# Performance work log

Hardware: AMD Instinct MI355X
Metric: run time of the kernel (lower is better)

## Reference

```python
import jax, jax.numpy as jnp
import numpy as np

EMBED_DIM = 512
NUM_HEADS = 8
DEPTH = EMBED_DIM // NUM_HEADS
B, S = 2, 4096


def setup_inputs() -> dict:
    key = jax.random.key(0)
    ks = jax.random.split(key, 11)
    s = 1.0 / np.sqrt(EMBED_DIM)
    return {
        "q": jax.random.normal(ks[0], (B, S, EMBED_DIM), jnp.float32),
        "k": jax.random.normal(ks[1], (B, S, EMBED_DIM), jnp.float32),
        "v": jax.random.normal(ks[2], (B, S, EMBED_DIM), jnp.float32),
        "mask": jnp.zeros((B, 1, 1, S), jnp.float32),  # additive mask: 1=masked, 0=keep
        "Wq": jax.random.normal(ks[3], (EMBED_DIM, EMBED_DIM), jnp.float32) * s,
        "bq": jnp.zeros((EMBED_DIM,), jnp.float32),
        "Wk": jax.random.normal(ks[4], (EMBED_DIM, EMBED_DIM), jnp.float32) * s,
        "bk": jnp.zeros((EMBED_DIM,), jnp.float32),
        "Wv": jax.random.normal(ks[5], (EMBED_DIM, EMBED_DIM), jnp.float32) * s,
        "bv": jnp.zeros((EMBED_DIM,), jnp.float32),
        "Wo": jax.random.normal(ks[6], (EMBED_DIM, EMBED_DIM), jnp.float32) * s,
        "bo": jnp.zeros((EMBED_DIM,), jnp.float32),
    }


def _split_heads(x):
    b, s, _ = x.shape
    return x.reshape(b, s, NUM_HEADS, DEPTH).transpose(0, 2, 1, 3)  # [B,H,S,D]


def reference(q, k, v, mask, Wq, bq, Wk, bk, Wv, bv, Wo, bo):
    qh = _split_heads(q @ Wq + bq)
    kh = _split_heads(k @ Wk + bk)
    vh = _split_heads(v @ Wv + bv)
    logits = jnp.einsum("bhqd,bhkd->bhqk", qh, kh) / jnp.sqrt(jnp.float32(DEPTH))
    logits = logits + mask * -1e9
    attn = jax.nn.softmax(logits, axis=-1)
    out = jnp.einsum("bhqk,bhkd->bhqd", attn, vh)
    out = out.transpose(0, 2, 1, 3).reshape(q.shape[0], -1, EMBED_DIM)
    return out @ Wo + bo
```

## Files before the change

### kernel.cpp

```cpp
#include <hip/hip_runtime.h>
#include <stdint.h>

typedef __bf16 bf16;
typedef bf16 bf16x8 __attribute__((ext_vector_type(8)));
typedef float f32x4 __attribute__((ext_vector_type(4)));
typedef float f32x16 __attribute__((ext_vector_type(16)));

#define EMBED 512
#define NHEAD 8
#define DEPTH 64
#define BATCH 2
#define SEQ 4096
#define M_TOTAL (BATCH * SEQ)
#define KVH 2048
#define NT (KVH / 64)

#define LOG2E 1.44269504f
#define QSCALE (0.125f * LOG2E)
#define MASKC (-1.0e9f * LOG2E)
#define DEFER_THR 10.0f

__device__ __forceinline__ void gload16(const void* g, void* l) {
  __builtin_amdgcn_global_load_lds((const __attribute__((address_space(1))) unsigned*)g,
                                   (__attribute__((address_space(3))) unsigned*)l, 16, 0, 0);
}
__device__ __forceinline__ uint32_t cvtpk(float a, float b) {
  uint32_t r;
  asm volatile("v_cvt_pk_bf16_f32 %0, %1, %2" : "=v"(r) : "v"(a), "v"(b));
  return r;
}
__device__ __forceinline__ void plswap(uint32_t& a, uint32_t& b) {
  asm volatile("v_permlane32_swap_b32 %0, %1" : "+v"(a), "+v"(b));
}
__device__ __forceinline__ float vdup(float x) {
  float r;
  asm volatile("v_mov_b32 %0, %1" : "=v"(r) : "v"(x));
  return r;
}
__device__ __forceinline__ float cross_max(float x) {
  float a = x, b = vdup(x);
  asm volatile("v_permlane32_swap_b32 %0, %1" : "+v"(a), "+v"(b));
  return fmaxf(a, b);
}
__device__ __forceinline__ float cross_sum(float x) {
  float a = x, b = vdup(x);
  asm volatile("v_permlane32_swap_b32 %0, %1" : "+v"(a), "+v"(b));
  return a + b;
}
union U4 { uint32_t u[4]; bf16x8 v; };

__global__ __launch_bounds__(256) void cvt3(const float* __restrict__ q, const float* __restrict__ k,
                                            const float* __restrict__ v, bf16* __restrict__ oq,
                                            bf16* __restrict__ ok, bf16* __restrict__ ov) {
  int z = blockIdx.y;
  const float* in = z == 0 ? q : (z == 1 ? k : v);
  bf16* out = z == 0 ? oq : (z == 1 ? ok : ov);
  size_t i = ((size_t)blockIdx.x * 256 + threadIdx.x) * 8;
  float4 f0 = *(const float4*)(in + i);
  float4 f1 = *(const float4*)(in + i + 4);
  bf16x8 o;
  o[0] = (bf16)f0.x; o[1] = (bf16)f0.y; o[2] = (bf16)f0.z; o[3] = (bf16)f0.w;
  o[4] = (bf16)f1.x; o[5] = (bf16)f1.y; o[6] = (bf16)f1.z; o[7] = (bf16)f1.w;
  *(bf16x8*)(out + i) = o;
}

__global__ __launch_bounds__(256) void transpose4(const float* __restrict__ W0, const float* __restrict__ W1,
                                                  const float* __restrict__ W2, const float* __restrict__ W3,
                                                  bf16* __restrict__ T0, bf16* __restrict__ T1,
                                                  bf16* __restrict__ T2, bf16* __restrict__ T3) {
  int z = blockIdx.z;
  const float* W = z == 0 ? W0 : (z == 1 ? W1 : (z == 2 ? W2 : W3));
  bf16* WT = z == 0 ? T0 : (z == 1 ? T1 : (z == 2 ? T2 : T3));
  __shared__ float t[32][33];
  int k0 = blockIdx.x * 32, n0 = blockIdx.y * 32;
  int x = threadIdx.x & 31, y = threadIdx.x >> 5;
#pragma unroll
  for (int yy = y; yy < 32; yy += 8)
    t[yy][x] = W[(size_t)(k0 + yy) * EMBED + n0 + x];
  __syncthreads();
#pragma unroll
  for (int yy = y; yy < 32; yy += 8)
    WT[(size_t)(n0 + yy) * EMBED + k0 + x] = (bf16)t[x][yy];
}

__device__ __forceinline__ void gemm128_body(const bf16* __restrict__ A, const bf16* __restrict__ Bt,
                                             const float* __restrict__ bias, void* __restrict__ out,
                                             float scale, int mode) {
  __shared__ __align__(16) bf16 As[128 * 64];
  __shared__ __align__(16) bf16 Bs[128 * 64];
  int tid = threadIdx.x, lane = tid & 63, w = tid >> 6;
  int g = lane >> 4, r = lane & 15;
  int n0 = blockIdx.x * 128, m0 = blockIdx.y * 128;
  int wr = (w >> 1) * 64, wc = (w & 1) * 64;

  f32x4 acc[4][4];
#pragma unroll
  for (int m = 0; m < 4; m++)
#pragma unroll
    for (int n = 0; n < 4; n++)
#pragma unroll
      for (int i = 0; i < 4; i++) acc[m][n][i] = 0.f;

  size_t aoff[4], boff[4];
#pragma unroll
  for (int i = 0; i < 4; i++) {
    int u = w * 64 + lane + i * 256;
    int row = u >> 3, scs = (u & 7) ^ (row & 7);
    aoff[i] = (size_t)(m0 + row) * EMBED + scs * 8;
    boff[i] = (size_t)(n0 + row) * EMBED + scs * 8;
  }

  for (int k0 = 0; k0 < EMBED; k0 += 64) {
#pragma unroll
    for (int i = 0; i < 4; i++) {
      gload16(A + aoff[i] + k0, &As[(w + i * 4) * 512]);
      gload16(Bt + boff[i] + k0, &Bs[(w + i * 4) * 512]);
    }
    __syncthreads();
#pragma unroll
    for (int kk = 0; kk < 64; kk += 32) {
      bf16x8 af[4], bf_[4];
#pragma unroll
      for (int m = 0; m < 4; m++) {
        int row = wr + m * 16 + r;
        af[m] = *(const bf16x8*)&As[row * 64 + (((kk >> 3) + g) ^ (r & 7)) * 8];
      }
#pragma unroll
      for (int n = 0; n < 4; n++) {
        int col = wc + n * 16 + r;
        bf_[n] = *(const bf16x8*)&Bs[col * 64 + (((kk >> 3) + g) ^ (r & 7)) * 8];
      }
      __builtin_amdgcn_s_setprio(1);
#pragma unroll
      for (int m = 0; m < 4; m++)
#pragma unroll
        for (int n = 0; n < 4; n++)
          acc[m][n] = __builtin_amdgcn_mfma_f32_16x16x32_bf16(af[m], bf_[n], acc[m][n], 0, 0, 0);
      __builtin_amdgcn_s_setprio(0);
    }
    __syncthreads();
  }

#pragma unroll
  for (int n = 0; n < 4; n++) {
    int ncol = n0 + wc + n * 16 + r;
    float bv = bias[ncol];
#pragma unroll
    for (int m = 0; m < 4; m++)
#pragma unroll
      for (int v_ = 0; v_ < 4; v_++) {
        int mrow = m0 + wr + m * 16 + g * 4 + v_;
        float val = (acc[m][n][v_] + bv) * scale;
        if (mode == 2) {
          ((float*)out)[(size_t)mrow * EMBED + ncol] = val;
        } else {
          int b = mrow >> 12, s = mrow & (SEQ - 1);
          int h = ncol >> 6, d = ncol & 63;
          size_t idx = (mode == 0) ? ((((size_t)(b * NHEAD + h)) * SEQ + s) * DEPTH + d)
                                   : ((((size_t)(b * NHEAD + h)) * DEPTH + d) * SEQ + s);
          ((bf16*)out)[idx] = (bf16)val;
        }
      }
  }
}

__global__ __launch_bounds__(256, 2) void gemm_qkv(const bf16* __restrict__ Xq, const bf16* __restrict__ Xk,
                                                   const bf16* __restrict__ Xv, const bf16* __restrict__ Tq,
                                                   const bf16* __restrict__ Tk, const bf16* __restrict__ Tv,
                                                   const float* __restrict__ bq, const float* __restrict__ bk,
                                                   const float* __restrict__ bv, bf16* __restrict__ qh,
                                                   bf16* __restrict__ kh, bf16* __restrict__ vT) {
  int z = blockIdx.z;
  const bf16* A = z == 0 ? Xq : (z == 1 ? Xk : Xv);
  const bf16* Bt = z == 0 ? Tq : (z == 1 ? Tk : Tv);
  const float* bias = z == 0 ? bq : (z == 1 ? bk : bv);
  void* out = z == 0 ? (void*)qh : (z == 1 ? (void*)kh : (void*)vT);
  float scale = z == 0 ? QSCALE : 1.0f;
  int mode = z == 2 ? 1 : 0;
  gemm128_body(A, Bt, bias, out, scale, mode);
}

__global__ __launch_bounds__(256, 2) void gemm_o(const bf16* __restrict__ A, const bf16* __restrict__ Bt,
                                                 const float* __restrict__ bias, float* __restrict__ out) {
  gemm128_body(A, Bt, bias, out, 1.0f, 2);
}

__global__ __launch_bounds__(512, 2) void flash_attn(const bf16* __restrict__ qh,
                                                     const bf16* __restrict__ kh,
                                                     const bf16* __restrict__ vT,
                                                     const float* __restrict__ mask,
                                                     bf16* __restrict__ O) {
  __shared__ __align__(16) unsigned char smem[65536];
  __shared__ float Sm[4][64];
  __shared__ float Sl[4][64];
  bf16* KV = (bf16*)smem;

  int tid = threadIdx.x;
  int lane = tid & 63, w = tid >> 6;
  int l31 = lane & 31, hi = lane >> 5, l7 = lane & 7;
  int qs = w & 3, half = w >> 2;
  int bh = blockIdx.y, b = bh >> 3, h = bh & 7;
  int q0 = blockIdx.x * 256;
  const bf16* Qb = qh + (size_t)bh * SEQ * DEPTH;
  const bf16* Kb = kh + (size_t)bh * SEQ * DEPTH;
  const bf16* Vb = vT + (size_t)bh * DEPTH * SEQ;
  const float* maskb = mask + (size_t)b * SEQ + half * KVH;

  int srow = tid >> 3;
  int scs = (tid & 7) ^ (srow & 7);
  const bf16* kg0 = Kb + (size_t)srow * DEPTH + scs * 8;
  const bf16* vg0 = Vb + (size_t)srow * SEQ + scs * 8;
  int wofs = w * 512;

#define STAGE(buf, kv)                                                              \
  do {                                                                              \
    gload16(kg0 + (size_t)(kv)*DEPTH, KV + (buf)*16384 + wofs);                     \
    gload16(kg0 + (size_t)((kv) + KVH) * DEPTH, KV + (buf)*16384 + 4096 + wofs);    \
    gload16(vg0 + (kv), KV + (buf)*16384 + 8192 + wofs);                            \
    gload16(vg0 + ((kv) + KVH), KV + (buf)*16384 + 12288 + wofs);                   \
  } while (0)

  STAGE(0, 0);

  bf16x8 qf[2][4];
#pragma unroll
  for (int q2 = 0; q2 < 2; q2++) {
    const bf16* qp = Qb + (size_t)(q0 + qs * 64 + q2 * 32 + l31) * DEPTH + hi * 8;
#pragma unroll
    for (int s = 0; s < 4; s++) qf[q2][s] = *(const bf16x8*)(qp + s * 16);
  }

  f32x16 oacc[2][2];
#pragma unroll
  for (int q2 = 0; q2 < 2; q2++)
#pragma unroll
    for (int nb = 0; nb < 2; nb++)
#pragma unroll
      for (int i = 0; i < 16; i++) oacc[q2][nb][i] = 0.f;
  float mrun[2] = {-__builtin_inff(), -__builtin_inff()};
  float lrun[2] = {0.f, 0.f};

  __syncthreads();

  int cur = 0;
  for (int t = 0; t < NT; ++t) {
    int kv = t * 64;
    if (t + 1 < NT) STAGE(cur ^ 1, kv + 64);

    const bf16* Kcur = KV + cur * 16384 + half * 4096;
    const bf16* Vcur = KV + cur * 16384 + 8192 + half * 4096;

    f32x4 mf[2][4];
#pragma unroll
    for (int m2 = 0; m2 < 2; m2++)
#pragma unroll
      for (int g = 0; g < 4; g++)
        mf[m2][g] = *(const f32x4*)(maskb + kv + m2 * 32 + g * 8 + 4 * hi);

    bf16x8 kf[2][4];
#pragma unroll
    for (int m2 = 0; m2 < 2; m2++)
#pragma unroll
      for (int s = 0; s < 4; s++)
        kf[m2][s] = *(const bf16x8*)(Kcur + (m2 * 32 + l31) * 64 + (((s * 2 + hi) ^ l7) * 8));

    bf16x8 pa[2][4];
#pragma unroll
    for (int q2 = 0; q2 < 2; q2++) {
      f32x16 sacc[2];
#pragma unroll
      for (int m2 = 0; m2 < 2; m2++)
#pragma unroll
        for (int i = 0; i < 16; i++) sacc[m2][i] = 0.f;
      __builtin_amdgcn_s_setprio(1);
#pragma unroll
      for (int m2 = 0; m2 < 2; m2++)
#pragma unroll
        for (int s = 0; s < 4; s++)
          sacc[m2] = __builtin_amdgcn_mfma_f32_32x32x16_bf16(kf[m2][s], qf[q2][s], sacc[m2], 0, 0, 0);
      __builtin_amdgcn_s_setprio(0);

#pragma unroll
      for (int m2 = 0; m2 < 2; m2++)
#pragma unroll
        for (int g = 0; g < 4; g++)
#pragma unroll
          for (int i = 0; i < 4; i++)
            sacc[m2][4 * g + i] = fmaf(mf[m2][g][i], MASKC, sacc[m2][4 * g + i]);

      float tmx[16];
#pragma unroll
      for (int i = 0; i < 16; i++) tmx[i] = fmaxf(sacc[0][i], sacc[1][i]);
#pragma unroll
      for (int i = 0; i < 8; i++) tmx[i] = fmaxf(tmx[i], tmx[i + 8]);
#pragma unroll
      for (int i = 0; i < 4; i++) tmx[i] = fmaxf(tmx[i], tmx[i + 4]);
      float pmax = fmaxf(fmaxf(tmx[0], tmx[1]), fmaxf(tmx[2], tmx[3]));
      pmax = cross_max(pmax);

      if (__any(pmax > mrun[q2] + DEFER_THR)) {
        float mnew = fmaxf(mrun[q2], pmax);
        float alpha = exp2f(mrun[q2] - mnew);
        lrun[q2] *= alpha;
        mrun[q2] = mnew;
#pragma unroll
        for (int r = 0; r < 16; r++) {
          float af = __shfl(alpha, (r & 3) + 8 * (r >> 2) + 4 * hi);
          oacc[q2][0][r] *= af;
          oacc[q2][1][r] *= af;
        }
      }

      float p[32];
      float rsv[4] = {0.f, 0.f, 0.f, 0.f};
#pragma unroll
      for (int m2 = 0; m2 < 2; m2++)
#pragma unroll
        for (int i = 0; i < 16; i++) {
          float pv = __builtin_amdgcn_exp2f(sacc[m2][i] - mrun[q2]);
          p[m2 * 16 + i] = pv;
          rsv[i & 3] += pv;
        }
      float rsum = (rsv[0] + rsv[1]) + (rsv[2] + rsv[3]);
      lrun[q2] += cross_sum(rsum);

#pragma unroll
      for (int m2 = 0; m2 < 2; m2++) {
        uint32_t c0 = cvtpk(p[m2 * 16 + 0], p[m2 * 16 + 1]);
        uint32_t c1 = cvtpk(p[m2 * 16 + 2], p[m2 * 16 + 3]);
        uint32_t d0 = cvtpk(p[m2 * 16 + 4], p[m2 * 16 + 5]);
        uint32_t d1 = cvtpk(p[m2 * 16 + 6], p[m2 * 16 + 7]);
        plswap(c0, d0);
        plswap(c1, d1);
        U4 e; e.u[0] = c0; e.u[1] = c1; e.u[2] = d0; e.u[3] = d1;
        pa[q2][m2 * 2 + 0] = e.v;
        uint32_t c2 = cvtpk(p[m2 * 16 + 8], p[m2 * 16 + 9]);
        uint32_t c3 = cvtpk(p[m2 * 16 + 10], p[m2 * 16 + 11]);
        uint32_t d2 = cvtpk(p[m2 * 16 + 12], p[m2 * 16 + 13]);
        uint32_t d3 = cvtpk(p[m2 * 16 + 14], p[m2 * 16 + 15]);
        plswap(c2, d2);
        plswap(c3, d3);
        U4 o; o.u[0] = c2; o.u[1] = c3; o.u[2] = d2; o.u[3] = d3;
        pa[q2][m2 * 2 + 1] = o.v;
      }
    }

    __builtin_amdgcn_s_setprio(1);
#pragma unroll
    for (int nb = 0; nb < 2; nb++)
#pragma unroll
      for (int ks = 0; ks < 4; ks++) {
        bf16x8 vf = *(const bf16x8*)(Vcur + (nb * 32 + l31) * 64 + (((ks * 2 + hi) ^ l7) * 8));
        oacc[0][nb] = __builtin_amdgcn_mfma_f32_32x32x16_bf16(pa[0][ks], vf, oacc[0][nb], 0, 0, 0);
        oacc[1][nb] = __builtin_amdgcn_mfma_f32_32x32x16_bf16(pa[1][ks], vf, oacc[1][nb], 0, 0, 0);
      }
    __builtin_amdgcn_s_setprio(0);

    __syncthreads();
    cur ^= 1;
  }

  float* Oex = (float*)smem;
  if (half == 1) {
    if (hi == 0) {
#pragma unroll
      for (int q2 = 0; q2 < 2; q2++) {
        Sm[qs][q2 * 32 + l31] = mrun[q2];
        Sl[qs][q2 * 32 + l31] = lrun[q2];
      }
    }
    float* Op = Oex + qs * 4096;
#pragma unroll
    for (int q2 = 0; q2 < 2; q2++)
#pragma unroll
      for (int nb = 0; nb < 2; nb++)
#pragma unroll
        for (int r = 0; r < 16; r++) {
          int cr = (r & 3) + 8 * (r >> 2) + 4 * hi;
          Op[(q2 * 32 + cr) * 64 + nb * 32 + l31] = oacc[q2][nb][r];
        }
  }
  __syncthreads();
  if (half == 0) {
    float s0[2], s1[2];
#pragma unroll
    for (int q2 = 0; q2 < 2; q2++) {
      float m1 = Sm[qs][q2 * 32 + l31];
      float l1 = Sl[qs][q2 * 32 + l31];
      float mm = fmaxf(mrun[q2], m1);
      float e0 = exp2f(mrun[q2] - mm);
      float e1 = exp2f(m1 - mm);
      float inv = 1.0f / (lrun[q2] * e0 + l1 * e1);
      s0[q2] = e0 * inv;
      s1[q2] = e1 * inv;
    }
    float* Op = Oex + qs * 4096;
    bf16* Ob = O + ((size_t)(b * SEQ + q0 + qs * 64)) * EMBED + h * DEPTH + l31;
#pragma unroll
    for (int q2 = 0; q2 < 2; q2++)
#pragma unroll
      for (int nb = 0; nb < 2; nb++)
#pragma unroll
        for (int r = 0; r < 16; r++) {
          int cr = (r & 3) + 8 * (r >> 2) + 4 * hi;
          float a0 = __shfl(s0[q2], cr);
          float a1 = __shfl(s1[q2], cr);
          float o1 = Op[(q2 * 32 + cr) * 64 + nb * 32 + l31];
          Ob[(size_t)(q2 * 32 + cr) * EMBED + nb * 32] = (bf16)(oacc[q2][nb][r] * a0 + o1 * a1);
        }
  }
#undef STAGE
}

extern "C" void kernel_launch(void* const* d_in, const int* in_sizes, int n_in,
                              void* d_out, int out_size, void* d_ws, size_t ws_size,
                              hipStream_t stream) {
  (void)in_sizes; (void)n_in; (void)out_size; (void)ws_size;
  const float* q = (const float*)d_in[0];
  const float* k = (const float*)d_in[1];
  const float* v = (const float*)d_in[2];
  const float* mask = (const float*)d_in[3];
  const float* Wq = (const float*)d_in[4];
  const float* bq = (const float*)d_in[5];
  const float* Wk = (const float*)d_in[6];
  const float* bk = (const float*)d_in[7];
  const float* Wv = (const float*)d_in[8];
  const float* bv = (const float*)d_in[9];
  const float* Wo = (const float*)d_in[10];
  const float* bo = (const float*)d_in[11];

  const size_t NX = (size_t)M_TOTAL * EMBED;
  const size_t NW = (size_t)EMBED * EMBED;
  bf16* Xq = (bf16*)d_ws;
  bf16* Xk = Xq + NX;
  bf16* Xv = Xk + NX;
  bf16* WTq = Xv + NX;
  bf16* WTk = WTq + NW;
  bf16* WTv = WTk + NW;
  bf16* WTo = WTv + NW;
  bf16* qh = WTo + NW;
  bf16* kh = qh + NX;
  bf16* vT = kh + NX;
  bf16* Ow = vT + NX;

  cvt3<<<dim3(NX / 2048, 3), 256, 0, stream>>>(q, k, v, Xq, Xk, Xv);
  transpose4<<<dim3(16, 16, 4), 256, 0, stream>>>(Wq, Wk, Wv, Wo, WTq, WTk, WTv, WTo);

  gemm_qkv<<<dim3(EMBED / 128, M_TOTAL / 128, 3), 256, 0, stream>>>(
      Xq, Xk, Xv, WTq, WTk, WTv, bq, bk, bv, qh, kh, vT);

  flash_attn<<<dim3(SEQ / 256, BATCH * NHEAD), 512, 0, stream>>>(qh, kh, vT, mask, Ow);

  gemm_o<<<dim3(EMBED / 128, M_TOTAL / 128), 256, 0, stream>>>(Ow, WTo, bo, (float*)d_out);
}
```

Before: 251.9 us.

## Restructure flash attention to single KV pass per block, fuse prep kernels, remap blocks

Flash attention drops the split-KV design (two halves of 4 waves each merged via shared memory). Each block now has 4 waves walking the full sequence, with a 32KB double buffer unrolled into a templated tile step, mask folded into the MFMA accumulator init, and a simple final normalisation. Launch bounds move to 256 threads with 4 blocks per CU. The input cast and weight transpose kernels are fused into one launch, and GEMM and attention block indices are swizzled so neighbouring blocks spread across XCDs. The trade-off is twice as many KV iterations per wave against removing the cross-half merge, gaining occupancy and saving one launch.

```diff
diff --git a/kernel.cpp b/kernel.cpp
--- a/kernel.cpp
+++ b/kernel.cpp
@@ -12,8 +12,6 @@
 #define BATCH 2
 #define SEQ 4096
 #define M_TOTAL (BATCH * SEQ)
-#define KVH 2048
-#define NT (KVH / 64)
 
 #define LOG2E 1.44269504f
 #define QSCALE (0.125f * LOG2E)
@@ -47,40 +45,46 @@
   asm volatile("v_permlane32_swap_b32 %0, %1" : "+v"(a), "+v"(b));
   return a + b;
 }
+__device__ __forceinline__ float max3f(float a, float b, float c) {
+  return fmaxf(fmaxf(a, b), c);
+}
 union U4 { uint32_t u[4]; bf16x8 v; };
 
-__global__ __launch_bounds__(256) void cvt3(const float* __restrict__ q, const float* __restrict__ k,
+__global__ __launch_bounds__(256) void prep(const float* __restrict__ q, const float* __restrict__ k,
                                             const float* __restrict__ v, bf16* __restrict__ oq,
-                                            bf16* __restrict__ ok, bf16* __restrict__ ov) {
+                                            bf16* __restrict__ ok, bf16* __restrict__ ov,
+                                            const float* __restrict__ W0, const float* __restrict__ W1,
+                                            const float* __restrict__ W2, const float* __restrict__ W3,
+                                            bf16* __restrict__ T0, bf16* __restrict__ T1,
+                                            bf16* __restrict__ T2, bf16* __restrict__ T3) {
+  __shared__ float t[32][33];
   int z = blockIdx.y;
-  const float* in = z == 0 ? q : (z == 1 ? k : v);
-  bf16* out = z == 0 ? oq : (z == 1 ? ok : ov);
-  size_t i = ((size_t)blockIdx.x * 256 + threadIdx.x) * 8;
-  float4 f0 = *(const float4*)(in + i);
-  float4 f1 = *(const float4*)(in + i + 4);
-  bf16x8 o;
-  o[0] = (bf16)f0.x; o[1] = (bf16)f0.y; o[2] = (bf16)f0.z; o[3] = (bf16)f0.w;
-  o[4] = (bf16)f1.x; o[5] = (bf16)f1.y; o[6] = (bf16)f1.z; o[7] = (bf16)f1.w;
-  *(bf16x8*)(out + i) = o;
-}
-
-__global__ __launch_bounds__(256) void transpose4(const float* __restrict__ W0, const float* __restrict__ W1,
-                                                  const float* __restrict__ W2, const float* __restrict__ W3,
-                                                  bf16* __restrict__ T0, bf16* __restrict__ T1,
-                                                  bf16* __restrict__ T2, bf16* __restrict__ T3) {
-  int z = blockIdx.z;
-  const float* W = z == 0 ? W0 : (z == 1 ? W1 : (z == 2 ? W2 : W3));
-  bf16* WT = z == 0 ? T0 : (z == 1 ? T1 : (z == 2 ? T2 : T3));
-  __shared__ float t[32][33];
-  int k0 = blockIdx.x * 32, n0 = blockIdx.y * 32;
-  int x = threadIdx.x & 31, y = threadIdx.x >> 5;
-#pragma unroll
-  for (int yy = y; yy < 32; yy += 8)
-    t[yy][x] = W[(size_t)(k0 + yy) * EMBED + n0 + x];
-  __syncthreads();
-#pragma unroll
-  for (int yy = y; yy < 32; yy += 8)
-    WT[(size_t)(n0 + yy) * EMBED + k0 + x] = (bf16)t[x][yy];
+  if (z < 3) {
+    const float* in = z == 0 ? q : (z == 1 ? k : v);
+    bf16* out = z == 0 ? oq : (z == 1 ? ok : ov);
+    size_t i = ((size_t)blockIdx.x * 256 + threadIdx.x) * 8;
+    float4 f0 = *(const float4*)(in + i);
+    float4 f1 = *(const float4*)(in + i + 4);
+    bf16x8 o;
+    o[0] = (bf16)f0.x; o[1] = (bf16)f0.y; o[2] = (bf16)f0.z; o[3] = (bf16)f0.w;
+    o[4] = (bf16)f1.x; o[5] = (bf16)f1.y; o[6] = (bf16)f1.z; o[7] = (bf16)f1.w;
+    *(bf16x8*)(out + i) = o;
+  } else {
+    int bx = blockIdx.x;
+    if (bx >= 1024) return;
+    int wsel = bx >> 8, rem = bx & 255;
+    const float* W = wsel == 0 ? W0 : (wsel == 1 ? W1 : (wsel == 2 ? W2 : W3));
+    bf16* WT = wsel == 0 ? T0 : (wsel == 1 ? T1 : (wsel == 2 ? T2 : T3));
+    int k0 = (rem >> 4) * 32, n0 = (rem & 15) * 32;
+    int x = threadIdx.x & 31, y = threadIdx.x >> 5;
+#pragma unroll
+    for (int yy = y; yy < 32; yy += 8)
+      t[yy][x] = W[(size_t)(k0 + yy) * EMBED + n0 + x];
+    __syncthreads();
+#pragma unroll
+    for (int yy = y; yy < 32; yy += 8)
+      WT[(size_t)(n0 + yy) * EMBED + k0 + x] = (bf16)t[x][yy];
+  }
 }
 
 __device__ __forceinline__ void gemm128_body(const bf16* __restrict__ A, const bf16* __restrict__ Bt,
@@ -90,7 +94,9 @@
   __shared__ __align__(16) bf16 Bs[128 * 64];
   int tid = threadIdx.x, lane = tid & 63, w = tid >> 6;
   int g = lane >> 4, r = lane & 15;
-  int n0 = blockIdx.x * 128, m0 = blockIdx.y * 128;
+  int orig = blockIdx.y * gridDim.x + blockIdx.x;
+  int wid = (orig & 7) * 32 + (orig >> 3);
+  int n0 = (wid & 3) * 128, m0 = (wid >> 2) * 128;
   int wr = (w >> 1) * 64, wc = (w & 1) * 64;
 
   f32x4 acc[4][4];
@@ -185,47 +191,157 @@
   gemm128_body(A, Bt, bias, out, 1.0f, 2);
 }
 
-__global__ __launch_bounds__(512, 2) void flash_attn(const bf16* __restrict__ qh,
+template <int BUF>
+__device__ __forceinline__ void tile_step(const char* rb, const int (&va)[4],
+                                          const bf16* kg0, const bf16* vg0, char* kvb,
+                                          const float* maskb, int kv, bool stage_next,
+                                          const bf16x8 (&qf)[2][4], f32x16 (&oacc)[2][2],
+                                          float (&mrun)[2], float (&lrun)[2], int hi) {
+  if (stage_next) {
+    int nkv = kv + 64;
+    gload16(kg0 + (size_t)nkv * DEPTH, kvb + (BUF ^ 1) * 8192);
+    gload16(kg0 + (size_t)(nkv + 32) * DEPTH, kvb + (BUF ^ 1) * 8192 + 4096);
+    gload16(vg0 + nkv, kvb + 16384 + (BUF ^ 1) * 8192);
+    gload16(vg0 + 32 * SEQ + nkv, kvb + 16384 + (BUF ^ 1) * 8192 + 4096);
+  }
+  f32x16 minit[2];
+#pragma unroll
+  for (int m2 = 0; m2 < 2; m2++)
+#pragma unroll
+    for (int g = 0; g < 4; g++) {
+      f32x4 f = *(const f32x4*)(maskb + kv + m2 * 32 + g * 8 + 4 * hi);
+#pragma unroll
+      for (int i = 0; i < 4; i++) minit[m2][4 * g + i] = f[i] * MASKC;
+    }
+  bf16x8 kf[2][4];
+#pragma unroll
+  for (int m2 = 0; m2 < 2; m2++)
+#pragma unroll
+    for (int s = 0; s < 4; s++)
+      kf[m2][s] = *(const bf16x8*)(rb + va[s] + BUF * 8192 + m2 * 4096);
+
+  bf16x8 pa[2][4];
+#pragma unroll
+  for (int q2 = 0; q2 < 2; q2++) {
+    f32x16 s0 = minit[0], s1 = minit[1];
+    __builtin_amdgcn_s_setprio(1);
+#pragma unroll
+    for (int s = 0; s < 4; s++) {
+      s0 = __builtin_amdgcn_mfma_f32_32x32x16_bf16(kf[0][s], qf[q2][s], s0, 0, 0, 0);
+      s1 = __builtin_amdgcn_mfma_f32_32x32x16_bf16(kf[1][s], qf[q2][s], s1, 0, 0, 0);
+    }
+    __builtin_amdgcn_s_setprio(0);
+
+    float mx[16];
+#pragma unroll
+    for (int i = 0; i < 16; i++) mx[i] = fmaxf(s0[i], s1[i]);
+    float u0 = max3f(mx[0], mx[1], mx[2]);
+    float u1 = max3f(mx[3], mx[4], mx[5]);
+    float u2 = max3f(mx[6], mx[7], mx[8]);
+    float u3 = max3f(mx[9], mx[10], mx[11]);
+    float u4 = max3f(mx[12], mx[13], mx[14]);
+    float pmax = fmaxf(max3f(u0, u1, u2), max3f(u3, u4, mx[15]));
+    pmax = cross_max(pmax);
+
+    if (__any(pmax > mrun[q2] + DEFER_THR)) {
+      float mnew = fmaxf(mrun[q2], pmax);
+      float alpha = exp2f(mrun[q2] - mnew);
+      lrun[q2] *= alpha;
+      mrun[q2] = mnew;
+#pragma unroll
+      for (int r = 0; r < 16; r++) {
+        float af = __shfl(alpha, (r & 3) + 8 * (r >> 2) + 4 * hi);
+        oacc[q2][0][r] *= af;
+        oacc[q2][1][r] *= af;
+      }
+    }
+
+    float p[32];
+    float rsv[4] = {0.f, 0.f, 0.f, 0.f};
+#pragma unroll
+    for (int i = 0; i < 16; i++) {
+      p[i] = __builtin_amdgcn_exp2f(s0[i] - mrun[q2]);
+      rsv[i & 3] += p[i];
+    }
+#pragma unroll
+    for (int i = 0; i < 16; i++) {
+      p[16 + i] = __builtin_amdgcn_exp2f(s1[i] - mrun[q2]);
+      rsv[i & 3] += p[16 + i];
+    }
+    lrun[q2] += cross_sum((rsv[0] + rsv[1]) + (rsv[2] + rsv[3]));
+
+#pragma unroll
+    for (int m2 = 0; m2 < 2; m2++) {
+      uint32_t c0 = cvtpk(p[m2 * 16 + 0], p[m2 * 16 + 1]);
+      uint32_t c1 = cvtpk(p[m2 * 16 + 2], p[m2 * 16 + 3]);
+      uint32_t d0 = cvtpk(p[m2 * 16 + 4], p[m2 * 16 + 5]);
+      uint32_t d1 = cvtpk(p[m2 * 16 + 6], p[m2 * 16 + 7]);
+      plswap(c0, d0);
+      plswap(c1, d1);
+      U4 e; e.u[0] = c0; e.u[1] = c1; e.u[2] = d0; e.u[3] = d1;
+      pa[q2][m2 * 2 + 0] = e.v;
+      uint32_t c2 = cvtpk(p[m2 * 16 + 8], p[m2 * 16 + 9]);
+      uint32_t c3 = cvtpk(p[m2 * 16 + 10], p[m2 * 16 + 11]);
+      uint32_t d2 = cvtpk(p[m2 * 16 + 12], p[m2 * 16 + 13]);
+      uint32_t d3 = cvtpk(p[m2 * 16 + 14], p[m2 * 16 + 15]);
+      plswap(c2, d2);
+      plswap(c3, d3);
+      U4 o; o.u[0] = c2; o.u[1] = c3; o.u[2] = d2; o.u[3] = d3;
+      pa[q2][m2 * 2 + 1] = o.v;
+    }
+  }
+
+  __builtin_amdgcn_s_setprio(1);
+#pragma unroll
+  for (int nb = 0; nb < 2; nb++)
+#pragma unroll
+    for (int ks = 0; ks < 4; ks++) {
+      bf16x8 vf = *(const bf16x8*)(rb + va[ks] + 16384 + BUF * 8192 + nb * 4096);
+      oacc[0][nb] = __builtin_amdgcn_mfma_f32_32x32x16_bf16(pa[0][ks], vf, oacc[0][nb], 0, 0, 0);
+      oacc[1][nb] = __builtin_amdgcn_mfma_f32_32x32x16_bf16(pa[1][ks], vf, oacc[1][nb], 0, 0, 0);
+    }
+  __builtin_amdgcn_s_setprio(0);
+  __syncthreads();
+}
+
+__global__ __launch_bounds__(256, 4) void flash_attn(const bf16* __restrict__ qh,
                                                      const bf16* __restrict__ kh,
                                                      const bf16* __restrict__ vT,
                                                      const float* __restrict__ mask,
                                                      bf16* __restrict__ O) {
-  __shared__ __align__(16) unsigned char smem[65536];
-  __shared__ float Sm[4][64];
-  __shared__ float Sl[4][64];
-  bf16* KV = (bf16*)smem;
-
-  int tid = threadIdx.x;
-  int lane = tid & 63, w = tid >> 6;
+  __shared__ __align__(16) unsigned char smem[32768];
+  int tid = threadIdx.x, lane = tid & 63, w = tid >> 6;
   int l31 = lane & 31, hi = lane >> 5, l7 = lane & 7;
-  int qs = w & 3, half = w >> 2;
-  int bh = blockIdx.y, b = bh >> 3, h = bh & 7;
-  int q0 = blockIdx.x * 256;
+  int orig = blockIdx.y * 16 + blockIdx.x;
+  int wid = (orig & 7) * 32 + (orig >> 3);
+  int qblk = wid & 15, bh = wid >> 4;
+  int b = bh >> 3, h = bh & 7;
+  int q0 = qblk * 256;
   const bf16* Qb = qh + (size_t)bh * SEQ * DEPTH;
   const bf16* Kb = kh + (size_t)bh * SEQ * DEPTH;
   const bf16* Vb = vT + (size_t)bh * DEPTH * SEQ;
-  const float* maskb = mask + (size_t)b * SEQ + half * KVH;
+  const float* maskb = mask + (size_t)b * SEQ;
 
   int srow = tid >> 3;
   int scs = (tid & 7) ^ (srow & 7);
   const bf16* kg0 = Kb + (size_t)srow * DEPTH + scs * 8;
   const bf16* vg0 = Vb + (size_t)srow * SEQ + scs * 8;
-  int wofs = w * 512;
-
-#define STAGE(buf, kv)                                                              \
-  do {                                                                              \
-    gload16(kg0 + (size_t)(kv)*DEPTH, KV + (buf)*16384 + wofs);                     \
-    gload16(kg0 + (size_t)((kv) + KVH) * DEPTH, KV + (buf)*16384 + 4096 + wofs);    \
-    gload16(vg0 + (kv), KV + (buf)*16384 + 8192 + wofs);                            \
-    gload16(vg0 + ((kv) + KVH), KV + (buf)*16384 + 12288 + wofs);                   \
-  } while (0)
-
-  STAGE(0, 0);
+  char* kvb = (char*)smem + w * 1024;
+  const char* rb = (const char*)smem;
+
+  int va[4];
+#pragma unroll
+  for (int s = 0; s < 4; s++) va[s] = l31 * 128 + (((s * 2 + hi) ^ l7) * 16);
+
+  gload16(kg0, kvb);
+  gload16(kg0 + (size_t)32 * DEPTH, kvb + 4096);
+  gload16(vg0, kvb + 16384);
+  gload16(vg0 + 32 * SEQ, kvb + 16384 + 4096);
 
   bf16x8 qf[2][4];
 #pragma unroll
   for (int q2 = 0; q2 < 2; q2++) {
-    const bf16* qp = Qb + (size_t)(q0 + qs * 64 + q2 * 32 + l31) * DEPTH + hi * 8;
+    const bf16* qp = Qb + (size_t)(q0 + w * 64 + q2 * 32 + l31) * DEPTH + hi * 8;
 #pragma unroll
     for (int s = 0; s < 4; s++) qf[q2][s] = *(const bf16x8*)(qp + s * 16);
   }
@@ -242,174 +358,24 @@
 
   __syncthreads();
 
-  int cur = 0;
-  for (int t = 0; t < NT; ++t) {
-    int kv = t * 64;
-    if (t + 1 < NT) STAGE(cur ^ 1, kv + 64);
-
-    const bf16* Kcur = KV + cur * 16384 + half * 4096;
-    const bf16* Vcur = KV + cur * 16384 + 8192 + half * 4096;
-
-    f32x4 mf[2][4];
-#pragma unroll
-    for (int m2 = 0; m2 < 2; m2++)
-#pragma unroll
-      for (int g = 0; g < 4; g++)
-        mf[m2][g] = *(const f32x4*)(maskb + kv + m2 * 32 + g * 8 + 4 * hi);
-
-    bf16x8 kf[2][4];
-#pragma unroll
-    for (int m2 = 0; m2 < 2; m2++)
-#pragma unroll
-      for (int s = 0; s < 4; s++)
-        kf[m2][s] = *(const bf16x8*)(Kcur + (m2 * 32 + l31) * 64 + (((s * 2 + hi) ^ l7) * 8));
-
-    bf16x8 pa[2][4];
-#pragma unroll
-    for (int q2 = 0; q2 < 2; q2++) {
-      f32x16 sacc[2];
-#pragma unroll
-      for (int m2 = 0; m2 < 2; m2++)
-#pragma unroll
-        for (int i = 0; i < 16; i++) sacc[m2][i] = 0.f;
-      __builtin_amdgcn_s_setprio(1);
-#pragma unroll
-      for (int m2 = 0; m2 < 2; m2++)
-#pragma unroll
-        for (int s = 0; s < 4; s++)
-          sacc[m2] = __builtin_amdgcn_mfma_f32_32x32x16_bf16(kf[m2][s], qf[q2][s], sacc[m2], 0, 0, 0);
-      __builtin_amdgcn_s_setprio(0);
-
-#pragma unroll
-      for (int m2 = 0; m2 < 2; m2++)
-#pragma unroll
-        for (int g = 0; g < 4; g++)
-#pragma unroll
-          for (int i = 0; i < 4; i++)
-            sacc[m2][4 * g + i] = fmaf(mf[m2][g][i], MASKC, sacc[m2][4 * g + i]);
-
-      float tmx[16];
-#pragma unroll
-      for (int i = 0; i < 16; i++) tmx[i] = fmaxf(sacc[0][i], sacc[1][i]);
-#pragma unroll
-      for (int i = 0; i < 8; i++) tmx[i] = fmaxf(tmx[i], tmx[i + 8]);
-#pragma unroll
-      for (int i = 0; i < 4; i++) tmx[i] = fmaxf(tmx[i], tmx[i + 4]);
-      float pmax = fmaxf(fmaxf(tmx[0], tmx[1]), fmaxf(tmx[2], tmx[3]));
-      pmax = cross_max(pmax);
-
-      if (__any(pmax > mrun[q2] + DEFER_THR)) {
-        float mnew = fmaxf(mrun[q2], pmax);
-        float alpha = exp2f(mrun[q2] - mnew);
-        lrun[q2] *= alpha;
-        mrun[q2] = mnew;
-#pragma unroll
-        for (int r = 0; r < 16; r++) {
-          float af = __shfl(alpha, (r & 3) + 8 * (r >> 2) + 4 * hi);
-          oacc[q2][0][r] *= af;
-          oacc[q2][1][r] *= af;
-        }
+#pragma unroll 1
+  for (int kv = 0; kv < SEQ; kv += 128) {
+    tile_step<0>(rb, va, kg0, vg0, kvb, maskb, kv, true, qf, oacc, mrun, lrun, hi);
+    tile_step<1>(rb, va, kg0, vg0, kvb, maskb, kv + 64, kv + 128 < SEQ, qf, oacc, mrun, lrun, hi);
+  }
+
+  float invl[2] = {1.0f / lrun[0], 1.0f / lrun[1]};
+  bf16* Ob = O + ((size_t)(b * SEQ + q0 + w * 64)) * EMBED + h * DEPTH + l31;
+#pragma unroll
+  for (int q2 = 0; q2 < 2; q2++)
+#pragma unroll
+    for (int nb = 0; nb < 2; nb++)
+#pragma unroll
+      for (int r = 0; r < 16; r++) {
+        int cr = (r & 3) + 8 * (r >> 2) + 4 * hi;
+        float iv = __shfl(invl[q2], cr);
+        Ob[(size_t)(q2 * 32 + cr) * EMBED + nb * 32] = (bf16)(oacc[q2][nb][r] * iv);
       }
-
-      float p[32];
-      float rsv[4] = {0.f, 0.f, 0.f, 0.f};
-#pragma unroll
-      for (int m2 = 0; m2 < 2; m2++)
-#pragma unroll
-        for (int i = 0; i < 16; i++) {
-          float pv = __builtin_amdgcn_exp2f(sacc[m2][i] - mrun[q2]);
-          p[m2 * 16 + i] = pv;
-          rsv[i & 3] += pv;
-        }
-      float rsum = (rsv[0] + rsv[1]) + (rsv[2] + rsv[3]);
-      lrun[q2] += cross_sum(rsum);
-
-#pragma unroll
-      for (int m2 = 0; m2 < 2; m2++) {
-        uint32_t c0 = cvtpk(p[m2 * 16 + 0], p[m2 * 16 + 1]);
-        uint32_t c1 = cvtpk(p[m2 * 16 + 2], p[m2 * 16 + 3]);
-        uint32_t d0 = cvtpk(p[m2 * 16 + 4], p[m2 * 16 + 5]);
-        uint32_t d1 = cvtpk(p[m2 * 16 + 6], p[m2 * 16 + 7]);
-        plswap(c0, d0);
-        plswap(c1, d1);
-        U4 e; e.u[0] = c0; e.u[1] = c1; e.u[2] = d0; e.u[3] = d1;
-        pa[q2][m2 * 2 + 0] = e.v;
-        uint32_t c2 = cvtpk(p[m2 * 16 + 8], p[m2 * 16 + 9]);
-        uint32_t c3 = cvtpk(p[m2 * 16 + 10], p[m2 * 16 + 11]);
-        uint32_t d2 = cvtpk(p[m2 * 16 + 12], p[m2 * 16 + 13]);
-        uint32_t d3 = cvtpk(p[m2 * 16 + 14], p[m2 * 16 + 15]);
-        plswap(c2, d2);
-        plswap(c3, d3);
-        U4 o; o.u[0] = c2; o.u[1] = c3; o.u[2] = d2; o.u[3] = d3;
-        pa[q2][m2 * 2 + 1] = o.v;
-      }
-    }
-
-    __builtin_amdgcn_s_setprio(1);
-#pragma unroll
-    for (int nb = 0; nb < 2; nb++)
-#pragma unroll
-      for (int ks = 0; ks < 4; ks++) {
-        bf16x8 vf = *(const bf16x8*)(Vcur + (nb * 32 + l31) * 64 + (((ks * 2 + hi) ^ l7) * 8));
-        oacc[0][nb] = __builtin_amdgcn_mfma_f32_32x32x16_bf16(pa[0][ks], vf, oacc[0][nb], 0, 0, 0);
-        oacc[1][nb] = __builtin_amdgcn_mfma_f32_32x32x16_bf16(pa[1][ks], vf, oacc[1][nb], 0, 0, 0);
-      }
-    __builtin_amdgcn_s_setprio(0);
-
-    __syncthreads();
-    cur ^= 1;
-  }
-
-  float* Oex = (float*)smem;
-  if (half == 1) {
-    if (hi == 0) {
-#pragma unroll
-      for (int q2 = 0; q2 < 2; q2++) {
-        Sm[qs][q2 * 32 + l31] = mrun[q2];
-        Sl[qs][q2 * 32 + l31] = lrun[q2];
-      }
-    }
-    float* Op = Oex + qs * 4096;
-#pragma unroll
-    for (int q2 = 0; q2 < 2; q2++)
-#pragma unroll
-      for (int nb = 0; nb < 2; nb++)
-#pragma unroll
-        for (int r = 0; r < 16; r++) {
-          int cr = (r & 3) + 8 * (r >> 2) + 4 * hi;
-          Op[(q2 * 32 + cr) * 64 + nb * 32 + l31] = oacc[q2][nb][r];
-        }
-  }
-  __syncthreads();
-  if (half == 0) {
-    float s0[2], s1[2];
-#pragma unroll
-    for (int q2 = 0; q2 < 2; q2++) {
-      float m1 = Sm[qs][q2 * 32 + l31];
-      float l1 = Sl[qs][q2 * 32 + l31];
-      float mm = fmaxf(mrun[q2], m1);
-      float e0 = exp2f(mrun[q2] - mm);
-      float e1 = exp2f(m1 - mm);
-      float inv = 1.0f / (lrun[q2] * e0 + l1 * e1);
-      s0[q2] = e0 * inv;
-      s1[q2] = e1 * inv;
-    }
-    float* Op = Oex + qs * 4096;
-    bf16* Ob = O + ((size_t)(b * SEQ + q0 + qs * 64)) * EMBED + h * DEPTH + l31;
-#pragma unroll
-    for (int q2 = 0; q2 < 2; q2++)
-#pragma unroll
-      for (int nb = 0; nb < 2; nb++)
-#pragma unroll
-        for (int r = 0; r < 16; r++) {
-          int cr = (r & 3) + 8 * (r >> 2) + 4 * hi;
-          float a0 = __shfl(s0[q2], cr);
-          float a1 = __shfl(s1[q2], cr);
-          float o1 = Op[(q2 * 32 + cr) * 64 + nb * 32 + l31];
-          Ob[(size_t)(q2 * 32 + cr) * EMBED + nb * 32] = (bf16)(oacc[q2][nb][r] * a0 + o1 * a1);
-        }
-  }
-#undef STAGE
 }
 
 extern "C" void kernel_launch(void* const* d_in, const int* in_sizes, int n_in,
@@ -443,13 +409,13 @@
   bf16* vT = kh + NX;
   bf16* Ow = vT + NX;
 
-  cvt3<<<dim3(NX / 2048, 3), 256, 0, stream>>>(q, k, v, Xq, Xk, Xv);
-  transpose4<<<dim3(16, 16, 4), 256, 0, stream>>>(Wq, Wk, Wv, Wo, WTq, WTk, WTv, WTo);
+  prep<<<dim3(NX / 2048, 4), 256, 0, stream>>>(q, k, v, Xq, Xk, Xv, Wq, Wk, Wv, Wo,
+                                               WTq, WTk, WTv, WTo);
 
   gemm_qkv<<<dim3(EMBED / 128, M_TOTAL / 128, 3), 256, 0, stream>>>(
       Xq, Xk, Xv, WTq, WTk, WTv, bq, bk, bv, qh, kh, vT);
 
-  flash_attn<<<dim3(SEQ / 256, BATCH * NHEAD), 512, 0, stream>>>(qh, kh, vT, mask, Ow);
+  flash_attn<<<dim3(16, 16), 256, 0, stream>>>(qh, kh, vT, mask, Ow);
 
   gemm_o<<<dim3(EMBED / 128, M_TOTAL / 128), 256, 0, stream>>>(Ow, WTo, bo, (float*)d_out);
 }
```

Result: slower. 743.2 us (+195.1%).
